# Kernel optimization log

Hardware: AMD Instinct MI355X
Metric: run time of the kernel (lower is better)

Reference implementation:

```python
import jax, jax.numpy as jnp
import numpy as np

N_NODES = 500000
N_EDGES = 5000000
IN_CH, OUT_CH = 16, 8


def setup_inputs() -> dict:
    key = jax.random.key(0)
    k1, k2, k3, k4, k5 = jax.random.split(key, 5)
    x = jax.random.normal(k1, (N_NODES, IN_CH), dtype=jnp.float32)
    src = jax.random.randint(k2, (N_EDGES,), 0, N_NODES, dtype=jnp.int64)
    dst = jax.random.randint(k3, (N_EDGES,), 0, N_NODES, dtype=jnp.int64)
    edge_index = jnp.stack([src, dst], axis=0)
    # PyG Linear: weight [out, in], Glorot init; GCNConv bias init zeros
    bound = np.sqrt(6.0 / (IN_CH + OUT_CH))
    W = jax.random.uniform(k4, (OUT_CH, IN_CH), dtype=jnp.float32, minval=-bound, maxval=bound)
    b = jnp.zeros((OUT_CH,), dtype=jnp.float32)
    return {"x": x, "edge_index": edge_index, "W": W, "b": b}


def reference(x, edge_index, W, b):
    """GCNConv(16, 8) with defaults: add_self_loops=True, normalize=True, bias.
    out = D^{-1/2} (A + I) D^{-1/2} X W^T + b, scatter by target index."""
    N = x.shape[0]
    loops = jnp.arange(N, dtype=edge_index.dtype)
    src = jnp.concatenate([edge_index[0], loops])  # [E + N]
    dst = jnp.concatenate([edge_index[1], loops])
    # degree of self-loop-augmented graph, accumulated at target nodes
    deg = jax.ops.segment_sum(jnp.ones(src.shape[0], dtype=x.dtype), dst, num_segments=N)
    dinv = jnp.where(deg > 0, jax.lax.rsqrt(deg), jnp.zeros_like(deg))
    norm = dinv[src] * dinv[dst]  # [E + N]
    h = x @ W.T  # [N, OUT_CH]
    msgs = norm[:, None] * h[src]  # gather + scale, [E + N, OUT_CH]
    out = jax.ops.segment_sum(msgs, dst, num_segments=N) + b
    return out
```

## Files before the change

kernel.cpp:

```cpp
#include <hip/hip_runtime.h>
#include <hip/hip_fp16.h>

#define IN_CH 16
#define OUT_CH 8

#define NT 256
#define EPT 24
#define TILE (NT*EPT)
#define NBUK 512
#define BSHIFT 10
#define BNODES 1024
#define BMASK 1023
#define SRCBITS 19
#define SRCMASK 0x7FFFF
#define CAP 12288
#define RPT 48

__global__ void __launch_bounds__(NT) k_bin(const int4* __restrict__ src4,
                                            const int4* __restrict__ dst4, int E,
                                            int* __restrict__ gcur,
                                            unsigned* __restrict__ gbuf) {
    __shared__ int hist[NBUK];
    __shared__ int lofs[NBUK];
    __shared__ int gofs[NBUK];
    __shared__ int scn[NT];
    __shared__ unsigned stage[TILE];
    __shared__ unsigned short posb[TILE];

    int t = threadIdx.x;
    long base = (long)blockIdx.x * TILE;
    int cnt = E - (int)base;
    if (cnt > TILE) cnt = TILE;

    for (int j = t; j < NBUK; j += NT) hist[j] = 0;
    __syncthreads();

    unsigned v[EPT];
    int bk[EPT];
    int rk[EPT];
#pragma unroll
    for (int k = 0; k < EPT / 4; k++) {
        int i4 = t + k * NT;
        if (4 * i4 < cnt) {
            int4 s = src4[base / 4 + i4];
            int4 d = dst4[base / 4 + i4];
            int ss[4] = {s.x, s.y, s.z, s.w};
            int dd[4] = {d.x, d.y, d.z, d.w};
#pragma unroll
            for (int j = 0; j < 4; j++) {
                int q = 4 * k + j;
                bk[q] = dd[j] >> BSHIFT;
                v[q] = ((unsigned)(dd[j] & BMASK) << SRCBITS) | (unsigned)ss[j];
                rk[q] = atomicAdd(&hist[bk[q]], 1);
            }
        } else {
#pragma unroll
            for (int j = 0; j < 4; j++) bk[4 * k + j] = -1;
        }
    }
    __syncthreads();

    int a0 = hist[2 * t], a1 = hist[2 * t + 1];
    int ts = a0 + a1;
    scn[t] = ts;
    __syncthreads();
    for (int d = 1; d < NT; d <<= 1) {
        int x = scn[t];
        int y = (t >= d) ? scn[t - d] : 0;
        __syncthreads();
        scn[t] = x + y;
        __syncthreads();
    }
    int excl = scn[t] - ts;
    lofs[2 * t] = excl;
    lofs[2 * t + 1] = excl + a0;
    if (a0 > 0) gofs[2 * t] = atomicAdd(&gcur[2 * t], a0) - excl;
    if (a1 > 0) gofs[2 * t + 1] = atomicAdd(&gcur[2 * t + 1], a1) - (excl + a0);
    __syncthreads();

#pragma unroll
    for (int k = 0; k < EPT; k++) {
        if (bk[k] >= 0) {
            int slot = lofs[bk[k]] + rk[k];
            stage[slot] = v[k];
            posb[slot] = (unsigned short)bk[k];
        }
    }
    __syncthreads();

#pragma unroll
    for (int k = 0; k < EPT; k++) {
        int idx = t + k * NT;
        if (idx < cnt) {
            int b2 = posb[idx];
            gbuf[(size_t)b2 * CAP + idx + gofs[b2]] = stage[idx];
        }
    }
}

__global__ void __launch_bounds__(NT) k_sort(unsigned* __restrict__ gbuf,
                                             const int* __restrict__ gcur,
                                             const float* __restrict__ x,
                                             const float* __restrict__ W,
                                             float* __restrict__ dinv,
                                             int* __restrict__ offs,
                                             int* __restrict__ cnts,
                                             uint4* __restrict__ hp16, int N) {
    __shared__ unsigned sorted[CAP];
    __shared__ int hist[BNODES];
    __shared__ int scn[NT];
    __shared__ float Ws[OUT_CH * IN_CH];

    int b = blockIdx.x, t = threadIdx.x;
    int cnt = gcur[b];
    unsigned* p = gbuf + (size_t)b * CAP;

    if (t < OUT_CH * IN_CH) Ws[t] = W[t];
    for (int j = t; j < BNODES; j += NT) hist[j] = 0;
    __syncthreads();

    unsigned v[RPT];
    int rk[RPT];
#pragma unroll
    for (int k = 0; k < RPT; k++) {
        int idx = t + k * NT;
        if (idx < cnt) {
            v[k] = p[idx];
            rk[k] = atomicAdd(&hist[v[k] >> SRCBITS], 1);
        }
    }
    __syncthreads();

    int h0 = hist[4 * t], h1 = hist[4 * t + 1], h2 = hist[4 * t + 2], h3 = hist[4 * t + 3];
    int ts = h0 + h1 + h2 + h3;
    scn[t] = ts;
    __syncthreads();
    for (int d = 1; d < NT; d <<= 1) {
        int xv = scn[t];
        int y = (t >= d) ? scn[t - d] : 0;
        __syncthreads();
        scn[t] = xv + y;
        __syncthreads();
    }
    int e0 = scn[t] - ts;
    int e1 = e0 + h0, e2 = e1 + h1, e3 = e2 + h2;
    hist[4 * t] = e0; hist[4 * t + 1] = e1; hist[4 * t + 2] = e2; hist[4 * t + 3] = e3;

    int nb = b << BSHIFT;
    int n0 = nb + 4 * t;
    int gofs2 = b * CAP;
    float di0 = rsqrtf(1.0f + (float)h0), di1 = rsqrtf(1.0f + (float)h1);
    float di2 = rsqrtf(1.0f + (float)h2), di3 = rsqrtf(1.0f + (float)h3);
    if (n0 + 3 < N) {
        *(int4*)(offs + n0) = make_int4(gofs2 + e0, gofs2 + e1, gofs2 + e2, gofs2 + e3);
        *(int4*)(cnts + n0) = make_int4(h0, h1, h2, h3);
        *(float4*)(dinv + n0) = make_float4(di0, di1, di2, di3);
    } else {
#pragma unroll
        for (int k = 0; k < 4; k++) {
            int n = n0 + k;
            if (n < N) {
                int hv = (k == 0) ? h0 : (k == 1) ? h1 : (k == 2) ? h2 : h3;
                int ev = (k == 0) ? e0 : (k == 1) ? e1 : (k == 2) ? e2 : e3;
                float dv = (k == 0) ? di0 : (k == 1) ? di1 : (k == 2) ? di2 : di3;
                offs[n] = gofs2 + ev;
                cnts[n] = hv;
                dinv[n] = dv;
            }
        }
    }
    __syncthreads();

#pragma unroll
    for (int k = 0; k < RPT; k++) {
        int idx = t + k * NT;
        if (idx < cnt) {
            int slot = hist[v[k] >> SRCBITS] + rk[k];
            sorted[slot] = v[k] & SRCMASK;
        }
    }
    __syncthreads();

    for (int i = t; i < cnt; i += NT) p[i] = sorted[i];

    float dis[4] = {di0, di1, di2, di3};
#pragma unroll
    for (int k = 0; k < 4; k++) {
        int n = n0 + k;
        if (n >= N) break;
        const float4* xp = (const float4*)(x + (size_t)n * IN_CH);
        float4 a0 = xp[0], a1 = xp[1], a2 = xp[2], a3 = xp[3];
        float xi[IN_CH] = {a0.x, a0.y, a0.z, a0.w, a1.x, a1.y, a1.z, a1.w,
                           a2.x, a2.y, a2.z, a2.w, a3.x, a3.y, a3.z, a3.w};
        float di = dis[k];
        float h[OUT_CH];
#pragma unroll
        for (int o = 0; o < OUT_CH; o++) {
            float s = 0.0f;
#pragma unroll
            for (int i = 0; i < IN_CH; i++) s += xi[i] * Ws[o * IN_CH + i];
            h[o] = s * di;
        }
        union { uint4 u; __half2 h2[4]; } pk;
        pk.h2[0] = __float22half2_rn(make_float2(h[0], h[1]));
        pk.h2[1] = __float22half2_rn(make_float2(h[2], h[3]));
        pk.h2[2] = __float22half2_rn(make_float2(h[4], h[5]));
        pk.h2[3] = __float22half2_rn(make_float2(h[6], h[7]));
        hp16[n] = pk.u;
    }
}

__device__ __forceinline__ void acc_add(float* a, uint4 g) {
    union { uint4 u; __half2 h2[4]; } pk;
    pk.u = g;
    float2 f0 = __half22float2(pk.h2[0]);
    float2 f1 = __half22float2(pk.h2[1]);
    float2 f2 = __half22float2(pk.h2[2]);
    float2 f3 = __half22float2(pk.h2[3]);
    a[0] += f0.x; a[1] += f0.y; a[2] += f1.x; a[3] += f1.y;
    a[4] += f2.x; a[5] += f2.y; a[6] += f3.x; a[7] += f3.y;
}

__global__ void __launch_bounds__(NT) k_gather(const unsigned* __restrict__ gbuf,
                                               const int* __restrict__ offs,
                                               const int* __restrict__ cnts,
                                               const uint4* __restrict__ hp16,
                                               const float* __restrict__ dinv,
                                               const float* __restrict__ bias,
                                               float* __restrict__ out, int N) {
    int tid = blockIdx.x * blockDim.x + threadIdx.x;
    int n = tid >> 1;
    if (n >= N) return;
    int q = tid & 1;

    int beg = offs[n];
    int end = beg + cnts[n];

    float a[OUT_CH] = {0, 0, 0, 0, 0, 0, 0, 0};
    if (q == 0) {
        union { uint4 u; __half2 h2[4]; } pk;
        pk.u = hp16[n];
        float2 f0 = __half22float2(pk.h2[0]);
        float2 f1 = __half22float2(pk.h2[1]);
        float2 f2 = __half22float2(pk.h2[2]);
        float2 f3 = __half22float2(pk.h2[3]);
        a[0] = f0.x; a[1] = f0.y; a[2] = f1.x; a[3] = f1.y;
        a[4] = f2.x; a[5] = f2.y; a[6] = f3.x; a[7] = f3.y;
    }

    int e = beg + q;
    for (; e + 6 < end; e += 8) {
        unsigned s0 = gbuf[e], s1 = gbuf[e + 2], s2 = gbuf[e + 4], s3 = gbuf[e + 6];
        uint4 g0 = hp16[s0];
        uint4 g1 = hp16[s1];
        uint4 g2 = hp16[s2];
        uint4 g3 = hp16[s3];
        acc_add(a, g0); acc_add(a, g1); acc_add(a, g2); acc_add(a, g3);
    }
    for (; e < end; e += 2) {
        uint4 g0 = hp16[gbuf[e]];
        acc_add(a, g0);
    }

#pragma unroll
    for (int c = 0; c < OUT_CH; c++) a[c] += __shfl_xor(a[c], 1);

    float di = dinv[n];
    const float4* b4 = (const float4*)bias;
    float4 bb = b4[q];
    float4 o;
    o.x = a[4 * q + 0] * di + bb.x;
    o.y = a[4 * q + 1] * di + bb.y;
    o.z = a[4 * q + 2] * di + bb.z;
    o.w = a[4 * q + 3] * di + bb.w;
    ((float4*)(out + (size_t)n * OUT_CH))[q] = o;
}

extern "C" void kernel_launch(void* const* d_in, const int* in_sizes, int n_in,
                              void* d_out, int out_size, void* d_ws, size_t ws_size,
                              hipStream_t stream) {
    const float* x  = (const float*)d_in[0];
    const int*   ei = (const int*)d_in[1];
    const float* W  = (const float*)d_in[2];
    const float* b  = (const float*)d_in[3];
    float* out = (float*)d_out;

    const int N = in_sizes[0] / IN_CH;
    const int E = in_sizes[1] / 2;
    const int* src = ei;
    const int* dst = ei + E;

    const int nbuckets = (N + BNODES - 1) >> BSHIFT;

    int*      gcur = (int*)d_ws;
    float*    dinv = (float*)(gcur + NBUK);
    uint4*    hp16 = (uint4*)(dinv + N);
    unsigned* gbuf = (unsigned*)(hp16 + N);
    int*      offs = (int*)(gbuf + (size_t)NBUK * CAP);
    int*      cnts = offs + N;

    const int tiles = (E + TILE - 1) / TILE;
    dim3 blkG((2 * N + NT - 1) / NT);

    hipMemsetAsync(gcur, 0, NBUK * sizeof(int), stream);
    k_bin<<<tiles, NT, 0, stream>>>((const int4*)src, (const int4*)dst, E, gcur, gbuf);
    k_sort<<<nbuckets, NT, 0, stream>>>(gbuf, gcur, x, W, dinv, offs, cnts, hp16, N);
    k_gather<<<blkG, NT, 0, stream>>>(gbuf, offs, cnts, hp16, dinv, b, out, N);
}
```

Baseline: 230.1 us.

## Use wave-shuffle scans, vectorized sort I/O, smaller bucket cap, 4 lanes per node

Several changes land together. The multi-barrier shared-memory prefix scan in the bin and sort kernels becomes an intra-wave __shfl_up scan plus a small per-wave sum combine, cutting barrier count. The sort kernel now loads and writes back bucket entries as uint4, and the bucket capacity and registers per thread shrink (CAP 12288→11264, RPT 48→44) to reduce LDS and register use. The gather kernel now assigns four threads per node instead of two, raising parallelism for the irregular neighbor gathers at the cost of shorter per-thread loops and an extra shuffle reduction; the smaller capacity also narrows the margin against bucket overflow.

```diff
diff --git a/kernel.cpp b/kernel.cpp
--- a/kernel.cpp
+++ b/kernel.cpp
@@ -13,8 +13,8 @@
 #define BMASK 1023
 #define SRCBITS 19
 #define SRCMASK 0x7FFFF
-#define CAP 12288
-#define RPT 48
+#define CAP 11264
+#define RPT 44
 
 __global__ void __launch_bounds__(NT) k_bin(const int4* __restrict__ src4,
                                             const int4* __restrict__ dst4, int E,
@@ -23,7 +23,7 @@
     __shared__ int hist[NBUK];
     __shared__ int lofs[NBUK];
     __shared__ int gofs[NBUK];
-    __shared__ int scn[NT];
+    __shared__ int wsum[4];
     __shared__ unsigned stage[TILE];
     __shared__ unsigned short posb[TILE];
 
@@ -62,16 +62,20 @@
 
     int a0 = hist[2 * t], a1 = hist[2 * t + 1];
     int ts = a0 + a1;
-    scn[t] = ts;
-    __syncthreads();
-    for (int d = 1; d < NT; d <<= 1) {
-        int x = scn[t];
-        int y = (t >= d) ? scn[t - d] : 0;
-        __syncthreads();
-        scn[t] = x + y;
-        __syncthreads();
-    }
-    int excl = scn[t] - ts;
+    int lane = t & 63, wv = t >> 6;
+    int inc = ts;
+#pragma unroll
+    for (int d = 1; d < 64; d <<= 1) {
+        int y = __shfl_up(inc, d);
+        if (lane >= d) inc += y;
+    }
+    if (lane == 63) wsum[wv] = inc;
+    __syncthreads();
+    int wpre = 0;
+#pragma unroll
+    for (int w = 0; w < 4; w++) wpre += (w < wv) ? wsum[w] : 0;
+    int excl = wpre + inc - ts;
+
     lofs[2 * t] = excl;
     lofs[2 * t + 1] = excl + a0;
     if (a0 > 0) gofs[2 * t] = atomicAdd(&gcur[2 * t], a0) - excl;
@@ -108,7 +112,7 @@
                                              uint4* __restrict__ hp16, int N) {
     __shared__ unsigned sorted[CAP];
     __shared__ int hist[BNODES];
-    __shared__ int scn[NT];
+    __shared__ int wsum[4];
     __shared__ float Ws[OUT_CH * IN_CH];
 
     int b = blockIdx.x, t = threadIdx.x;
@@ -122,27 +126,36 @@
     unsigned v[RPT];
     int rk[RPT];
 #pragma unroll
-    for (int k = 0; k < RPT; k++) {
-        int idx = t + k * NT;
-        if (idx < cnt) {
-            v[k] = p[idx];
-            rk[k] = atomicAdd(&hist[v[k] >> SRCBITS], 1);
+    for (int k4 = 0; k4 < RPT / 4; k4++) {
+        int idx = 4 * t + k4 * 4 * NT;
+        uint4 vv = *(const uint4*)(p + idx);
+        unsigned vs[4] = {vv.x, vv.y, vv.z, vv.w};
+#pragma unroll
+        for (int j = 0; j < 4; j++) {
+            int k = 4 * k4 + j;
+            if (idx + j < cnt) {
+                v[k] = vs[j];
+                rk[k] = atomicAdd(&hist[v[k] >> SRCBITS], 1);
+            }
         }
     }
     __syncthreads();
 
     int h0 = hist[4 * t], h1 = hist[4 * t + 1], h2 = hist[4 * t + 2], h3 = hist[4 * t + 3];
     int ts = h0 + h1 + h2 + h3;
-    scn[t] = ts;
-    __syncthreads();
-    for (int d = 1; d < NT; d <<= 1) {
-        int xv = scn[t];
-        int y = (t >= d) ? scn[t - d] : 0;
-        __syncthreads();
-        scn[t] = xv + y;
-        __syncthreads();
-    }
-    int e0 = scn[t] - ts;
+    int lane = t & 63, wv = t >> 6;
+    int inc = ts;
+#pragma unroll
+    for (int d = 1; d < 64; d <<= 1) {
+        int y = __shfl_up(inc, d);
+        if (lane >= d) inc += y;
+    }
+    if (lane == 63) wsum[wv] = inc;
+    __syncthreads();
+    int wpre = 0;
+#pragma unroll
+    for (int w = 0; w < 4; w++) wpre += (w < wv) ? wsum[w] : 0;
+    int e0 = wpre + inc - ts;
     int e1 = e0 + h0, e2 = e1 + h1, e3 = e2 + h2;
     hist[4 * t] = e0; hist[4 * t + 1] = e1; hist[4 * t + 2] = e2; hist[4 * t + 3] = e3;
 
@@ -173,15 +186,29 @@
 
 #pragma unroll
     for (int k = 0; k < RPT; k++) {
-        int idx = t + k * NT;
-        if (idx < cnt) {
-            int slot = hist[v[k] >> SRCBITS] + rk[k];
-            sorted[slot] = v[k] & SRCMASK;
-        }
-    }
-    __syncthreads();
-
-    for (int i = t; i < cnt; i += NT) p[i] = sorted[i];
+        int idx = t + (k % 4) + (k / 4) * 4 * NT;
+        (void)idx;
+    }
+#pragma unroll
+    for (int k4 = 0; k4 < RPT / 4; k4++) {
+#pragma unroll
+        for (int j = 0; j < 4; j++) {
+            int k = 4 * k4 + j;
+            int idx = 4 * t + k4 * 4 * NT + j;
+            if (idx < cnt) {
+                int slot = hist[v[k] >> SRCBITS] + rk[k];
+                sorted[slot] = v[k] & SRCMASK;
+            }
+        }
+    }
+    __syncthreads();
+
+    int full = cnt & ~3;
+    for (int i = 4 * t; i < full; i += 4 * NT) {
+        uint4 sv = *(const uint4*)&sorted[i];
+        *(uint4*)(p + i) = sv;
+    }
+    for (int i = full + t; i < cnt; i += NT) p[i] = sorted[i];
 
     float dis[4] = {di0, di1, di2, di3};
 #pragma unroll
@@ -229,9 +256,9 @@
                                                const float* __restrict__ bias,
                                                float* __restrict__ out, int N) {
     int tid = blockIdx.x * blockDim.x + threadIdx.x;
-    int n = tid >> 1;
+    int n = tid >> 2;
     if (n >= N) return;
-    int q = tid & 1;
+    int q = tid & 3;
 
     int beg = offs[n];
     int end = beg + cnts[n];
@@ -249,31 +276,29 @@
     }
 
     int e = beg + q;
-    for (; e + 6 < end; e += 8) {
-        unsigned s0 = gbuf[e], s1 = gbuf[e + 2], s2 = gbuf[e + 4], s3 = gbuf[e + 6];
+    for (; e + 4 < end; e += 8) {
+        unsigned s0 = gbuf[e], s1 = gbuf[e + 4];
         uint4 g0 = hp16[s0];
         uint4 g1 = hp16[s1];
-        uint4 g2 = hp16[s2];
-        uint4 g3 = hp16[s3];
-        acc_add(a, g0); acc_add(a, g1); acc_add(a, g2); acc_add(a, g3);
-    }
-    for (; e < end; e += 2) {
+        acc_add(a, g0);
+        acc_add(a, g1);
+    }
+    if (e < end) {
         uint4 g0 = hp16[gbuf[e]];
         acc_add(a, g0);
     }
 
 #pragma unroll
-    for (int c = 0; c < OUT_CH; c++) a[c] += __shfl_xor(a[c], 1);
+    for (int c = 0; c < OUT_CH; c++) {
+        a[c] += __shfl_xor(a[c], 1);
+        a[c] += __shfl_xor(a[c], 2);
+    }
 
     float di = dinv[n];
-    const float4* b4 = (const float4*)bias;
-    float4 bb = b4[q];
-    float4 o;
-    o.x = a[4 * q + 0] * di + bb.x;
-    o.y = a[4 * q + 1] * di + bb.y;
-    o.z = a[4 * q + 2] * di + bb.z;
-    o.w = a[4 * q + 3] * di + bb.w;
-    ((float4*)(out + (size_t)n * OUT_CH))[q] = o;
+    float2 o;
+    o.x = a[2 * q + 0] * di + bias[2 * q + 0];
+    o.y = a[2 * q + 1] * di + bias[2 * q + 1];
+    ((float2*)(out + (size_t)n * OUT_CH))[q] = o;
 }
 
 extern "C" void kernel_launch(void* const* d_in, const int* in_sizes, int n_in,
@@ -300,7 +325,7 @@
     int*      cnts = offs + N;
 
     const int tiles = (E + TILE - 1) / TILE;
-    dim3 blkG((2 * N + NT - 1) / NT);
+    dim3 blkG((4 * (long)N + NT - 1) / NT);
 
     hipMemsetAsync(gcur, 0, NBUK * sizeof(int), stream);
     k_bin<<<tiles, NT, 0, stream>>>((const int4*)src, (const int4*)dst, E, gcur, gbuf);
```

Result: faster. 222.1 us (-3.5%).
